# Kernel optimization log

Hardware: AMD Instinct MI355X
Metric: run time of the kernel (lower is better)

Reference implementation:

```python
import jax, jax.numpy as jnp
import numpy as np

M = 19
DIM = 768
D = DIM // 2  # r=2 -> 384
EPS = 1e-5


def _bn_eval(h, gamma, beta):
    # eval-mode BatchNorm1d with running_mean=0, running_var=1
    return h * (gamma / jnp.sqrt(1.0 + EPS)) + beta


def setup_inputs() -> dict:
    key = jax.random.key(0)
    ks = jax.random.split(key, 24)
    s = 0.02
    inp = {
        "x": jax.random.normal(ks[0], (4096, M * DIM), jnp.float32),
        "g": jax.random.normal(ks[1], (4096, M * DIM), jnp.float32),
        # fc: Linear(768,384) -> ReLU -> BN(384) -> Linear(384,384)
        "fc1_W": jax.random.normal(ks[2], (D, DIM), jnp.float32) * s,
        "fc1_b": jnp.zeros((D,), jnp.float32),
        "bn1_g": jnp.ones((D,), jnp.float32),
        "bn1_b": jnp.zeros((D,), jnp.float32),
        "fc2_W": jax.random.normal(ks[3], (D, D), jnp.float32) * s,
        "fc2_b": jnp.zeros((D,), jnp.float32),
        # 19 branch Linears fcs: (d,d); g_fcs: (dim+d, dim)
        "fcs_W": jax.random.normal(ks[4], (M, D, D), jnp.float32) * s,
        "fcs_b": jnp.zeros((M, D), jnp.float32),
        "gfcs_W": jax.random.normal(ks[5], (M, DIM, DIM + D), jnp.float32) * s,
        "gfcs_b": jnp.zeros((M, DIM), jnp.float32),
        # classifier head (numpy_class=20 < 30): 768->128->32->20
        "l1_W": jax.random.normal(ks[6], (128, DIM), jnp.float32) * s,
        "l1_b": jnp.zeros((128,), jnp.float32),
        "bna_g": jnp.ones((128,), jnp.float32),
        "bna_b": jnp.zeros((128,), jnp.float32),
        "l2_W": jax.random.normal(ks[7], (32, 128), jnp.float32) * s,
        "l2_b": jnp.zeros((32,), jnp.float32),
        "bnb_g": jnp.ones((32,), jnp.float32),
        "bnb_b": jnp.zeros((32,), jnp.float32),
        "l3_W": jax.random.normal(ks[8], (20, 32), jnp.float32) * s,
        "l3_b": jnp.zeros((20,), jnp.float32),
    }
    return inp


def reference(x, g, fc1_W, fc1_b, bn1_g, bn1_b, fc2_W, fc2_b,
              fcs_W, fcs_b, gfcs_W, gfcs_b,
              l1_W, l1_b, bna_g, bna_b, l2_W, l2_b, bnb_g, bnb_b, l3_W, l3_b):
    bs = x.shape[0]
    x3 = x.reshape(bs, M, DIM)
    g3 = g.reshape(bs, M, DIM)

    # selective_ts_with_g
    fea_u = jnp.sum(x3, axis=1)                              # (bs, 768)
    h = jax.nn.relu(fea_u @ fc1_W.T + fc1_b)
    h = _bn_eval(h, bn1_g, bn1_b)
    fea_z = h @ fc2_W.T + fc2_b                              # (bs, 384)

    # 19 branch small GEMMs, batched
    vec = jnp.einsum('bd,mod->bmo', fea_z, fcs_W) + fcs_b    # (bs, 19, 384)
    cat = jnp.concatenate([vec, g3], axis=-1)                # (bs, 19, 1152)
    att = jnp.einsum('bmi,moi->bmo', cat, gfcs_W) + gfcs_b   # (bs, 19, 768)
    att = jax.nn.softmax(att, axis=1)                        # softmax over 19 branches
    fea_v = jnp.sum(x3 * att, axis=1)                        # (bs, 768)

    # classifier head
    h = jax.nn.relu(fea_v @ l1_W.T + l1_b)
    h = _bn_eval(h, bna_g, bna_b)
    h = jax.nn.relu(h @ l2_W.T + l2_b)
    h = _bn_eval(h, bnb_g, bnb_b)
    return h @ l3_W.T + l3_b                                 # (bs, 20)
```

## Files before the change

### kernel.cpp

```cpp
#include <hip/hip_runtime.h>


typedef unsigned short u16;
typedef unsigned int u32;
typedef long long i64;
typedef float f32x4 __attribute__((ext_vector_type(4)));
typedef __bf16 bf16x8 __attribute__((ext_vector_type(8)));

#define GPTR(p) ((const __attribute__((address_space(1))) void*)(p))
#define SPTR(p) ((__attribute__((address_space(3))) void*)(p))

__device__ __forceinline__ u16 f2bf(float f) {
    u32 u = __float_as_uint(f);
    u += 0x7fffu + ((u >> 16) & 1u);
    return (u16)(u >> 16);
}
__device__ __forceinline__ float bf2f(u16 h) {
    return __uint_as_float(((u32)h) << 16);
}
__device__ __forceinline__ u32 pk2(float a, float b) {
    return (u32)f2bf(a) | ((u32)f2bf(b) << 16);
}

#define BNRS 0.9999950000374997f

#define EPI_NONE    0
#define EPI_BIAS    1
#define EPI_RELU_BN 2

template <int EPI>
__global__ __launch_bounds__(256)
void gemm_bf16_kernel(const u16* __restrict__ A, i64 Abat, int lda,
                      const u16* __restrict__ B, i64 Bbat, int ldb,
                      const float* __restrict__ bias,
                      const float* __restrict__ bnG, const float* __restrict__ bnB,
                      u16* __restrict__ C, i64 Cbat, int ldc, int K)
{
    constexpr int BK = 32;
    __shared__ __align__(16) u16 lA[128 * BK];
    __shared__ __align__(16) u16 lB[128 * BK];

    const int z    = blockIdx.z;
    const int tid  = threadIdx.x;
    const int wave = tid >> 6;
    const int lane = tid & 63;
    const int bm   = blockIdx.x * 128;
    const int bn   = blockIdx.y * 128;
    const int wm   = (wave >> 1) * 64;
    const int wn   = (wave & 1) * 64;
    const int rl   = lane & 15;
    const int qk   = (lane >> 4) * 8;

    f32x4 acc[4][4] = {};

    const u16* Ab = A + (size_t)z * Abat + (size_t)bm * lda;
    const u16* Bb = B + (size_t)z * Bbat + (size_t)bn * ldb;

    for (int k0 = 0; k0 < K; k0 += BK) {
#pragma unroll
        for (int r = 0; r < 2; ++r) {
            const int c   = r * 256 + wave * 64 + lane;
            const int row = c >> 2;
            const int kc  = (c & 3) << 3;
            const u16* sa = Ab + (size_t)row * lda + (k0 + kc);
            const u16* sb = Bb + (size_t)row * ldb + (k0 + kc);
            __builtin_amdgcn_global_load_lds(GPTR(sa), SPTR(&lA[(r * 256 + wave * 64) * 8]), 16, 0, 0);
            __builtin_amdgcn_global_load_lds(GPTR(sb), SPTR(&lB[(r * 256 + wave * 64) * 8]), 16, 0, 0);
        }
        __syncthreads();

        bf16x8 af[4], bfr[4];
#pragma unroll
        for (int i = 0; i < 4; ++i) af[i]  = *(const bf16x8*)&lA[(wm + i * 16 + rl) * BK + qk];
#pragma unroll
        for (int j = 0; j < 4; ++j) bfr[j] = *(const bf16x8*)&lB[(wn + j * 16 + rl) * BK + qk];
#pragma unroll
        for (int i = 0; i < 4; ++i)
#pragma unroll
            for (int j = 0; j < 4; ++j)
                acc[i][j] = __builtin_amdgcn_mfma_f32_16x16x32_bf16(af[i], bfr[j], acc[i][j], 0, 0, 0);
        __syncthreads();
    }

    u16* Cb = C + (size_t)z * Cbat;
    const int q4 = (lane >> 4) * 4;
#pragma unroll
    for (int j = 0; j < 4; ++j) {
        const int col = bn + wn + j * 16 + rl;
        float bsv = 0.f, scl = 1.f, sft = 0.f;
        if constexpr (EPI != EPI_NONE) bsv = bias[col];
        if constexpr (EPI == EPI_RELU_BN) { scl = bnG[col] * BNRS; sft = bnB[col]; }
#pragma unroll
        for (int i = 0; i < 4; ++i) {
            const int row0 = bm + wm + i * 16 + q4;
#pragma unroll
            for (int r = 0; r < 4; ++r) {
                float v = acc[i][j][r];
                if constexpr (EPI != EPI_NONE) v += bsv;
                if constexpr (EPI == EPI_RELU_BN) v = fmaxf(v, 0.f) * scl + sft;
                Cb[(size_t)(row0 + r) * ldc + col] = f2bf(v);
            }
        }
    }
}

__global__ __launch_bounds__(256)
void att_gemm_a_kernel(const u16* __restrict__ feaz, const u16* __restrict__ gb,
                       const u16* __restrict__ W, const float* __restrict__ bc,
                       u16* __restrict__ att)
{
    constexpr int BK = 32, K = 1152;
    __shared__ __align__(16) u16 lA[128 * BK];
    __shared__ __align__(16) u16 lB[128 * BK];

    const int m    = blockIdx.z;
    const int tid  = threadIdx.x;
    const int wave = tid >> 6;
    const int lane = tid & 63;
    const int bm   = blockIdx.x * 128;
    const int bn   = blockIdx.y * 128;
    const int wm   = (wave >> 1) * 64;
    const int wn   = (wave & 1) * 64;
    const int rl   = lane & 15;
    const int qk   = (lane >> 4) * 8;

    f32x4 acc[4][4] = {};

    const u16* A1 = feaz + (size_t)bm * 384;
    const u16* A2 = gb + (size_t)bm * 14592 + m * 768;
    const u16* Bb = W + (size_t)m * 884736 + (size_t)bn * K;

    for (int k0 = 0; k0 < K; k0 += BK) {
#pragma unroll
        for (int r = 0; r < 2; ++r) {
            const int c   = r * 256 + wave * 64 + lane;
            const int row = c >> 2;
            const int kc  = (c & 3) << 3;
            const u16* sa = (k0 < 384)
                ? A1 + (size_t)row * 384 + (k0 + kc)
                : A2 + (size_t)row * 14592 + (k0 - 384 + kc);
            const u16* sb = Bb + (size_t)row * K + (k0 + kc);
            __builtin_amdgcn_global_load_lds(GPTR(sa), SPTR(&lA[(r * 256 + wave * 64) * 8]), 16, 0, 0);
            __builtin_amdgcn_global_load_lds(GPTR(sb), SPTR(&lB[(r * 256 + wave * 64) * 8]), 16, 0, 0);
        }
        __syncthreads();

        bf16x8 af[4], bfr[4];
#pragma unroll
        for (int i = 0; i < 4; ++i) af[i]  = *(const bf16x8*)&lA[(wm + i * 16 + rl) * BK + qk];
#pragma unroll
        for (int j = 0; j < 4; ++j) bfr[j] = *(const bf16x8*)&lB[(wn + j * 16 + rl) * BK + qk];
#pragma unroll
        for (int i = 0; i < 4; ++i)
#pragma unroll
            for (int j = 0; j < 4; ++j)
                acc[i][j] = __builtin_amdgcn_mfma_f32_16x16x32_bf16(af[i], bfr[j], acc[i][j], 0, 0, 0);
        __syncthreads();
    }

    const int q4 = (lane >> 4) * 4;
#pragma unroll
    for (int j = 0; j < 4; ++j) {
        const int col = bn + wn + j * 16 + rl;
        const float bsv = bc[m * 768 + col];
#pragma unroll
        for (int i = 0; i < 4; ++i) {
            const int row0 = bm + wm + i * 16 + q4;
#pragma unroll
            for (int r = 0; r < 4; ++r)
                att[(size_t)(row0 + r) * 14592 + m * 768 + col] = f2bf(acc[i][j][r] + bsv);
        }
    }
}

__global__ __launch_bounds__(256)
void att_gemm_b_kernel(const u16* __restrict__ feaz, const float* __restrict__ g,
                       const u16* __restrict__ W, const float* __restrict__ bc,
                       u16* __restrict__ att)
{
    constexpr int BK = 32, K = 1152;
    __shared__ __align__(16) u16 lA[128 * BK];
    __shared__ __align__(16) u16 lB[128 * BK];

    const int m    = blockIdx.z;
    const int tid  = threadIdx.x;
    const int wave = tid >> 6;
    const int lane = tid & 63;
    const int bm   = blockIdx.x * 128;
    const int bn   = blockIdx.y * 128;
    const int wm   = (wave >> 1) * 64;
    const int wn   = (wave & 1) * 64;
    const int rl   = lane & 15;
    const int qk   = (lane >> 4) * 8;

    f32x4 acc[4][4] = {};

    const u16* A1 = feaz + (size_t)bm * 384;
    const float* Ag = g + (size_t)bm * 14592 + m * 768;
    const u16* Bb = W + (size_t)m * 884736 + (size_t)bn * K;

    for (int k0 = 0; k0 < K; k0 += BK) {
        if (k0 < 384) {
#pragma unroll
            for (int r = 0; r < 2; ++r) {
                const int c   = r * 256 + wave * 64 + lane;
                const int row = c >> 2;
                const int kc  = (c & 3) << 3;
                const u16* sa = A1 + (size_t)row * 384 + (k0 + kc);
                __builtin_amdgcn_global_load_lds(GPTR(sa), SPTR(&lA[(r * 256 + wave * 64) * 8]), 16, 0, 0);
            }
        } else {
#pragma unroll
            for (int r = 0; r < 2; ++r) {
                const int c   = r * 256 + tid;
                const int row = c >> 2;
                const int kc  = (c & 3) << 3;
                const float* sf = Ag + (size_t)row * 14592 + (k0 - 384 + kc);
                const float4 f0 = *(const float4*)sf;
                const float4 f1 = *(const float4*)(sf + 4);
                uint4 pk;
                pk.x = pk2(f0.x, f0.y);  pk.y = pk2(f0.z, f0.w);
                pk.z = pk2(f1.x, f1.y);  pk.w = pk2(f1.z, f1.w);
                *(uint4*)&lA[c * 8] = pk;
            }
        }
#pragma unroll
        for (int r = 0; r < 2; ++r) {
            const int c   = r * 256 + wave * 64 + lane;
            const int row = c >> 2;
            const int kc  = (c & 3) << 3;
            const u16* sb = Bb + (size_t)row * K + (k0 + kc);
            __builtin_amdgcn_global_load_lds(GPTR(sb), SPTR(&lB[(r * 256 + wave * 64) * 8]), 16, 0, 0);
        }
        __syncthreads();

        bf16x8 af[4], bfr[4];
#pragma unroll
        for (int i = 0; i < 4; ++i) af[i]  = *(const bf16x8*)&lA[(wm + i * 16 + rl) * BK + qk];
#pragma unroll
        for (int j = 0; j < 4; ++j) bfr[j] = *(const bf16x8*)&lB[(wn + j * 16 + rl) * BK + qk];
#pragma unroll
        for (int i = 0; i < 4; ++i)
#pragma unroll
            for (int j = 0; j < 4; ++j)
                acc[i][j] = __builtin_amdgcn_mfma_f32_16x16x32_bf16(af[i], bfr[j], acc[i][j], 0, 0, 0);
        __syncthreads();
    }

    const int q4 = (lane >> 4) * 4;
#pragma unroll
    for (int j = 0; j < 4; ++j) {
        const int col = bn + wn + j * 16 + rl;
        const float bsv = bc[m * 768 + col];
#pragma unroll
        for (int i = 0; i < 4; ++i) {
            const int row0 = bm + wm + i * 16 + q4;
#pragma unroll
            for (int r = 0; r < 4; ++r)
                att[(size_t)(row0 + r) * 14592 + m * 768 + col] = f2bf(acc[i][j][r] + bsv);
        }
    }
}


__global__ __launch_bounds__(256)
void cvt_flat_kernel(const float* __restrict__ s0, const float* __restrict__ s1,
                     const float* __restrict__ s2,
                     u16* __restrict__ d0, u16* __restrict__ d1, u16* __restrict__ d2)
{
    const int i = blockIdx.x * 256 + threadIdx.x;
    const float* s; u16* d; int off;
    if (i < 36864)      { s = s0; d = d0; off = i; }
    else if (i < 55296) { s = s1; d = d1; off = i - 36864; }
    else                { s = s2; d = d2; off = i - 55296; }
    const float4 f0 = *(const float4*)(s + off * 8);
    const float4 f1 = *(const float4*)(s + off * 8 + 4);
    uint4 pk; pk.x = pk2(f0.x, f0.y); pk.y = pk2(f0.z, f0.w);
    pk.z = pk2(f1.x, f1.y); pk.w = pk2(f1.z, f1.w);
    *(uint4*)(d + off * 8) = pk;
}

__global__ __launch_bounds__(256)
void cvt_gfcs_kernel(const float* __restrict__ gfcs, u16* __restrict__ w1,
                     u16* __restrict__ geff)
{
    const int i = blockIdx.x * 256 + threadIdx.x;
    const int r = i / 144, c = i - r * 144;
    const float* s = gfcs + (size_t)r * 1152 + c * 8;
    const float4 f0 = *(const float4*)s;
    const float4 f1 = *(const float4*)(s + 4);
    uint4 pk; pk.x = pk2(f0.x, f0.y); pk.y = pk2(f0.z, f0.w);
    pk.z = pk2(f1.x, f1.y); pk.w = pk2(f1.z, f1.w);
    u16* d = (c < 48) ? (w1 + (size_t)r * 384 + c * 8)
                      : (geff + (size_t)r * 1152 + c * 8);
    *(uint4*)d = pk;
}

__global__ __launch_bounds__(256)
void cvt_fcsT_kernel(const float* __restrict__ fcs, u16* __restrict__ fcswT)
{
    const int i = blockIdx.x * 256 + threadIdx.x;
    const int m = i / 18432, rem = i - m * 18432;
    const int d = rem / 48, e8 = (rem - d * 48) * 8;
    const float* s = fcs + (size_t)m * 147456 + (size_t)e8 * 384 + d;
    float f[8];
#pragma unroll
    for (int j = 0; j < 8; ++j) f[j] = s[j * 384];
    uint4 pk; pk.x = pk2(f[0], f[1]); pk.y = pk2(f[2], f[3]);
    pk.z = pk2(f[4], f[5]); pk.w = pk2(f[6], f[7]);
    *(uint4*)(fcswT + (size_t)m * 147456 + (size_t)d * 384 + e8) = pk;
}

__global__ __launch_bounds__(256)
void cvt_g_kernel(const float* __restrict__ g, u16* __restrict__ gb)
{
    const size_t i = ((size_t)blockIdx.x * 256 + threadIdx.x) * 8;
    const float4 f0 = *(const float4*)(g + i);
    const float4 f1 = *(const float4*)(g + i + 4);
    uint4 pk; pk.x = pk2(f0.x, f0.y); pk.y = pk2(f0.z, f0.w);
    pk.z = pk2(f1.x, f1.y); pk.w = pk2(f1.z, f1.w);
    *(uint4*)(gb + i) = pk;
}

__global__ __launch_bounds__(256)
void bc_kernel(const float* __restrict__ gfcs, const float* __restrict__ gfcs_b,
               const float* __restrict__ fcs_b, float* __restrict__ bc)
{
    const int widx = blockIdx.x * 4 + (threadIdx.x >> 6);
    const int lane = threadIdx.x & 63;
    const int m = widx / 768, o = widx - m * 768;
    const float* wr = gfcs + (size_t)m * 884736 + (size_t)o * 1152;
    const float* fb = fcs_b + m * 384;
    float a = 0.f;
#pragma unroll
    for (int t = 0; t < 6; ++t) a += wr[lane + t * 64] * fb[lane + t * 64];
#pragma unroll
    for (int off = 32; off > 0; off >>= 1) a += __shfl_down(a, off, 64);
    if (lane == 0) bc[widx] = gfcs_b[widx] + a;
}

__global__ __launch_bounds__(192)
void feau_kernel(const float* __restrict__ x, u16* __restrict__ feau)
{
    const int b = blockIdx.x;
    const int o = threadIdx.x * 4;
    const float* xp = x + (size_t)b * 14592 + o;
    float4 s = {0.f, 0.f, 0.f, 0.f};
#pragma unroll
    for (int m = 0; m < 19; ++m) {
        const float4 v = *(const float4*)(xp + m * 768);
        s.x += v.x; s.y += v.y; s.z += v.z; s.w += v.w;
    }
    ushort4 r; r.x = f2bf(s.x); r.y = f2bf(s.y); r.z = f2bf(s.z); r.w = f2bf(s.w);
    *(ushort4*)(feau + (size_t)b * 768 + o) = r;
}

__global__ __launch_bounds__(192)
void softmax_feav_kernel(const u16* __restrict__ att, const float* __restrict__ x,
                         u16* __restrict__ feav)
{
    const int b = blockIdx.x;
    const int o = threadIdx.x * 4;
    const u16* ap   = att + (size_t)b * 14592 + o;
    const float* xp = x   + (size_t)b * 14592 + o;
    float4 l[19];
    float4 mx = {-1e30f, -1e30f, -1e30f, -1e30f};
#pragma unroll
    for (int m = 0; m < 19; ++m) {
        const ushort4 u = *(const ushort4*)(ap + m * 768);
        l[m].x = bf2f(u.x); l[m].y = bf2f(u.y); l[m].z = bf2f(u.z); l[m].w = bf2f(u.w);
        mx.x = fmaxf(mx.x, l[m].x); mx.y = fmaxf(mx.y, l[m].y);
        mx.z = fmaxf(mx.z, l[m].z); mx.w = fmaxf(mx.w, l[m].w);
    }
    float4 s = {0.f, 0.f, 0.f, 0.f};
#pragma unroll
    for (int m = 0; m < 19; ++m) {
        l[m].x = __expf(l[m].x - mx.x); s.x += l[m].x;
        l[m].y = __expf(l[m].y - mx.y); s.y += l[m].y;
        l[m].z = __expf(l[m].z - mx.z); s.z += l[m].z;
        l[m].w = __expf(l[m].w - mx.w); s.w += l[m].w;
    }
    const float4 inv = {1.f / s.x, 1.f / s.y, 1.f / s.z, 1.f / s.w};
    float4 a = {0.f, 0.f, 0.f, 0.f};
#pragma unroll
    for (int m = 0; m < 19; ++m) {
        const float4 v = *(const float4*)(xp + m * 768);
        a.x += v.x * l[m].x; a.y += v.y * l[m].y;
        a.z += v.z * l[m].z; a.w += v.w * l[m].w;
    }
    ushort4 r;
    r.x = f2bf(a.x * inv.x); r.y = f2bf(a.y * inv.y);
    r.z = f2bf(a.z * inv.z); r.w = f2bf(a.w * inv.w);
    *(ushort4*)(feav + (size_t)b * 768 + o) = r;
}

__global__ __launch_bounds__(256)
void l2_kernel(const u16* __restrict__ h1, const float* __restrict__ W,
               const float* __restrict__ bias, const float* __restrict__ bg,
               const float* __restrict__ bb, float* __restrict__ h2)
{
    const int idx = blockIdx.x * 256 + threadIdx.x;
    const int b = idx >> 5, n = idx & 31;
    const u16* hp  = h1 + (size_t)b * 128;
    const float* wp = W + n * 128;
    float a = bias[n];
#pragma unroll 8
    for (int k = 0; k < 128; ++k) a += bf2f(hp[k]) * wp[k];
    a = fmaxf(a, 0.f) * (bg[n] * BNRS) + bb[n];
    h2[idx] = a;
}

__global__ __launch_bounds__(256)
void l3_kernel(const float* __restrict__ h2, const float* __restrict__ W,
               const float* __restrict__ bias, float* __restrict__ out)
{
    const int idx = blockIdx.x * 256 + threadIdx.x;
    const int b = idx / 20, n = idx - b * 20;
    const float* hp = h2 + (size_t)b * 32;
    const float* wp = W + n * 32;
    float a = bias[n];
#pragma unroll
    for (int k = 0; k < 32; ++k) a += hp[k] * wp[k];
    out[idx] = a;
}

extern "C" void kernel_launch(void* const* d_in, const int* in_sizes, int n_in,
                              void* d_out, int out_size, void* d_ws, size_t ws_size,
                              hipStream_t stream)
{
    const float* x      = (const float*)d_in[0];
    const float* g      = (const float*)d_in[1];
    const float* fc1_W  = (const float*)d_in[2];
    const float* fc1_b  = (const float*)d_in[3];
    const float* bn1_g  = (const float*)d_in[4];
    const float* bn1_b  = (const float*)d_in[5];
    const float* fc2_W  = (const float*)d_in[6];
    const float* fc2_b  = (const float*)d_in[7];
    const float* fcs_W  = (const float*)d_in[8];
    const float* fcs_b  = (const float*)d_in[9];
    const float* gfcs_W = (const float*)d_in[10];
    const float* gfcs_b = (const float*)d_in[11];
    const float* l1_W   = (const float*)d_in[12];
    const float* l1_b   = (const float*)d_in[13];
    const float* bna_g  = (const float*)d_in[14];
    const float* bna_b  = (const float*)d_in[15];
    const float* l2_W   = (const float*)d_in[16];
    const float* l2_b   = (const float*)d_in[17];
    const float* bnb_g  = (const float*)d_in[18];
    const float* bnb_b  = (const float*)d_in[19];
    const float* l3_W   = (const float*)d_in[20];
    const float* l3_b   = (const float*)d_in[21];
    float* out = (float*)d_out;
    (void)in_sizes; (void)n_in; (void)out_size;

    char* w = (char*)d_ws;
    size_t off = 0;
    auto alloc = [&](size_t bytes) { void* p = w + off; off += (bytes + 255) & ~(size_t)255; return p; };
    u16* fc1w  = (u16*)alloc(294912ull * 2);
    u16* fc2w  = (u16*)alloc(147456ull * 2);
    u16* l1w   = (u16*)alloc(98304ull * 2);
    u16* fcswT = (u16*)alloc(2801664ull * 2);
    u16* w1bf  = (u16*)alloc(5603328ull * 2);
    u16* geff  = (u16*)alloc(16809984ull * 2);
    float* bcb = (float*)alloc(14592ull * 4);
    u16* feau  = (u16*)alloc(3145728ull * 2);
    u16* hbuf  = (u16*)alloc(1572864ull * 2);
    u16* feaz  = (u16*)alloc(1572864ull * 2);
    u16* attb  = (u16*)alloc(59768832ull * 2);
    u16* feav  = (u16*)alloc(3145728ull * 2);
    u16* h1b   = (u16*)alloc(524288ull * 2);
    float* h2f = (float*)alloc(131072ull * 4);
    u16* gbf   = (u16*)alloc(59768832ull * 2);
    const bool useA = (ws_size >= off);

    cvt_flat_kernel<<<264, 256, 0, stream>>>(fc1_W, fc2_W, l1_W, fc1w, fc2w, l1w);
    cvt_gfcs_kernel<<<8208, 256, 0, stream>>>(gfcs_W, w1bf, geff);
    cvt_fcsT_kernel<<<1368, 256, 0, stream>>>(fcs_W, fcswT);
    bc_kernel<<<3648, 256, 0, stream>>>(gfcs_W, gfcs_b, fcs_b, bcb);
    gemm_bf16_kernel<EPI_NONE><<<dim3(6, 3, 19), 256, 0, stream>>>(
        w1bf, 294912, 384, fcswT, 147456, 384, nullptr, nullptr, nullptr,
        geff, 884736, 1152, 384);
    if (useA) cvt_g_kernel<<<29184, 256, 0, stream>>>(g, gbf);

    feau_kernel<<<4096, 192, 0, stream>>>(x, feau);
    gemm_bf16_kernel<EPI_RELU_BN><<<dim3(32, 3), 256, 0, stream>>>(
        feau, 0, 768, fc1w, 0, 768, fc1_b, bn1_g, bn1_b, hbuf, 0, 384, 768);
    gemm_bf16_kernel<EPI_BIAS><<<dim3(32, 3), 256, 0, stream>>>(
        hbuf, 0, 384, fc2w, 0, 384, fc2_b, nullptr, nullptr, feaz, 0, 384, 384);

    if (useA)
        att_gemm_a_kernel<<<dim3(32, 6, 19), 256, 0, stream>>>(feaz, gbf, geff, bcb, attb);
    else
        att_gemm_b_kernel<<<dim3(32, 6, 19), 256, 0, stream>>>(feaz, g, geff, bcb, attb);
    softmax_feav_kernel<<<4096, 192, 0, stream>>>(attb, x, feav);

    gemm_bf16_kernel<EPI_RELU_BN><<<dim3(32, 1), 256, 0, stream>>>(
        feav, 0, 768, l1w, 0, 768, l1_b, bna_g, bna_b, h1b, 0, 128, 768);
    l2_kernel<<<512, 256, 0, stream>>>(h1b, l2_W, l2_b, bnb_g, bnb_b, h2f);
    l3_kernel<<<320, 256, 0, stream>>>(h2f, l3_W, l3_b, out);
}
```

Before: 930.6 us.

## Fuse g fp32-to-bf16 conversion into attention GEMM via async LDS loads

Drops the separate pass that converts g to a bf16 workspace copy. The attention GEMM now loads raw fp32 g tiles into LDS with async global-to-LDS loads and converts them to bf16 while building MFMA fragments. This removes one full read and write of the 4096x14592 g tensor, at the cost of a larger LDS footprint and conversion work inside the GEMM loop. It also replaces the fcs transpose with an LDS-tiled transpose and fuses the l2 and l3 head layers into a single kernel.

```diff
diff --git a/kernel.cpp b/kernel.cpp
--- a/kernel.cpp
+++ b/kernel.cpp
@@ -105,13 +105,14 @@
 }
 
 __global__ __launch_bounds__(256)
-void att_gemm_a_kernel(const u16* __restrict__ feaz, const u16* __restrict__ gb,
-                       const u16* __restrict__ W, const float* __restrict__ bc,
-                       u16* __restrict__ att)
+void att_gemm_kernel(const u16* __restrict__ feaz, const float* __restrict__ g,
+                     const u16* __restrict__ W, const float* __restrict__ bc,
+                     u16* __restrict__ att)
 {
     constexpr int BK = 32, K = 1152;
     __shared__ __align__(16) u16 lA[128 * BK];
     __shared__ __align__(16) u16 lB[128 * BK];
+    __shared__ __align__(16) float lG[128 * BK];
 
     const int m    = blockIdx.z;
     const int tid  = threadIdx.x;
@@ -126,78 +127,9 @@
 
     f32x4 acc[4][4] = {};
 
-    const u16* A1 = feaz + (size_t)bm * 384;
-    const u16* A2 = gb + (size_t)bm * 14592 + m * 768;
-    const u16* Bb = W + (size_t)m * 884736 + (size_t)bn * K;
-
-    for (int k0 = 0; k0 < K; k0 += BK) {
-#pragma unroll
-        for (int r = 0; r < 2; ++r) {
-            const int c   = r * 256 + wave * 64 + lane;
-            const int row = c >> 2;
-            const int kc  = (c & 3) << 3;
-            const u16* sa = (k0 < 384)
-                ? A1 + (size_t)row * 384 + (k0 + kc)
-                : A2 + (size_t)row * 14592 + (k0 - 384 + kc);
-            const u16* sb = Bb + (size_t)row * K + (k0 + kc);
-            __builtin_amdgcn_global_load_lds(GPTR(sa), SPTR(&lA[(r * 256 + wave * 64) * 8]), 16, 0, 0);
-            __builtin_amdgcn_global_load_lds(GPTR(sb), SPTR(&lB[(r * 256 + wave * 64) * 8]), 16, 0, 0);
-        }
-        __syncthreads();
-
-        bf16x8 af[4], bfr[4];
-#pragma unroll
-        for (int i = 0; i < 4; ++i) af[i]  = *(const bf16x8*)&lA[(wm + i * 16 + rl) * BK + qk];
-#pragma unroll
-        for (int j = 0; j < 4; ++j) bfr[j] = *(const bf16x8*)&lB[(wn + j * 16 + rl) * BK + qk];
-#pragma unroll
-        for (int i = 0; i < 4; ++i)
-#pragma unroll
-            for (int j = 0; j < 4; ++j)
-                acc[i][j] = __builtin_amdgcn_mfma_f32_16x16x32_bf16(af[i], bfr[j], acc[i][j], 0, 0, 0);
-        __syncthreads();
-    }
-
-    const int q4 = (lane >> 4) * 4;
-#pragma unroll
-    for (int j = 0; j < 4; ++j) {
-        const int col = bn + wn + j * 16 + rl;
-        const float bsv = bc[m * 768 + col];
-#pragma unroll
-        for (int i = 0; i < 4; ++i) {
-            const int row0 = bm + wm + i * 16 + q4;
-#pragma unroll
-            for (int r = 0; r < 4; ++r)
-                att[(size_t)(row0 + r) * 14592 + m * 768 + col] = f2bf(acc[i][j][r] + bsv);
-        }
-    }
-}
-
-__global__ __launch_bounds__(256)
-void att_gemm_b_kernel(const u16* __restrict__ feaz, const float* __restrict__ g,
-                       const u16* __restrict__ W, const float* __restrict__ bc,
-                       u16* __restrict__ att)
-{
-    constexpr int BK = 32, K = 1152;
-    __shared__ __align__(16) u16 lA[128 * BK];
-    __shared__ __align__(16) u16 lB[128 * BK];
-
-    const int m    = blockIdx.z;
-    const int tid  = threadIdx.x;
-    const int wave = tid >> 6;
-    const int lane = tid & 63;
-    const int bm   = blockIdx.x * 128;
-    const int bn   = blockIdx.y * 128;
-    const int wm   = (wave >> 1) * 64;
-    const int wn   = (wave & 1) * 64;
-    const int rl   = lane & 15;
-    const int qk   = (lane >> 4) * 8;
-
-    f32x4 acc[4][4] = {};
-
-    const u16* A1 = feaz + (size_t)bm * 384;
+    const u16*  A1 = feaz + (size_t)bm * 384;
     const float* Ag = g + (size_t)bm * 14592 + m * 768;
-    const u16* Bb = W + (size_t)m * 884736 + (size_t)bn * K;
+    const u16*  Bb = W + (size_t)m * 884736 + (size_t)bn * K;
 
     for (int k0 = 0; k0 < K; k0 += BK) {
         if (k0 < 384) {
@@ -211,17 +143,12 @@
             }
         } else {
 #pragma unroll
-            for (int r = 0; r < 2; ++r) {
-                const int c   = r * 256 + tid;
-                const int row = c >> 2;
-                const int kc  = (c & 3) << 3;
-                const float* sf = Ag + (size_t)row * 14592 + (k0 - 384 + kc);
-                const float4 f0 = *(const float4*)sf;
-                const float4 f1 = *(const float4*)(sf + 4);
-                uint4 pk;
-                pk.x = pk2(f0.x, f0.y);  pk.y = pk2(f0.z, f0.w);
-                pk.z = pk2(f1.x, f1.y);  pk.w = pk2(f1.z, f1.w);
-                *(uint4*)&lA[c * 8] = pk;
+            for (int r = 0; r < 4; ++r) {
+                const int c   = r * 256 + wave * 64 + lane;
+                const int row = c >> 3;
+                const int kc  = (c & 7) << 2;
+                const float* sg = Ag + (size_t)row * 14592 + (k0 - 384 + kc);
+                __builtin_amdgcn_global_load_lds(GPTR(sg), SPTR(&lG[(r * 256 + wave * 64) * 4]), 16, 0, 0);
             }
         }
 #pragma unroll
@@ -235,8 +162,21 @@
         __syncthreads();
 
         bf16x8 af[4], bfr[4];
-#pragma unroll
-        for (int i = 0; i < 4; ++i) af[i]  = *(const bf16x8*)&lA[(wm + i * 16 + rl) * BK + qk];
+        if (k0 < 384) {
+#pragma unroll
+            for (int i = 0; i < 4; ++i) af[i] = *(const bf16x8*)&lA[(wm + i * 16 + rl) * BK + qk];
+        } else {
+#pragma unroll
+            for (int i = 0; i < 4; ++i) {
+                const float* p = &lG[(wm + i * 16 + rl) * BK + qk];
+                const float4 p0 = *(const float4*)p;
+                const float4 p1 = *(const float4*)(p + 4);
+                union { bf16x8 v; uint4 u; } cv;
+                cv.u.x = pk2(p0.x, p0.y); cv.u.y = pk2(p0.z, p0.w);
+                cv.u.z = pk2(p1.x, p1.y); cv.u.w = pk2(p1.z, p1.w);
+                af[i] = cv.v;
+            }
+        }
 #pragma unroll
         for (int j = 0; j < 4; ++j) bfr[j] = *(const bf16x8*)&lB[(wn + j * 16 + rl) * BK + qk];
 #pragma unroll
@@ -297,29 +237,33 @@
 }
 
 __global__ __launch_bounds__(256)
-void cvt_fcsT_kernel(const float* __restrict__ fcs, u16* __restrict__ fcswT)
-{
-    const int i = blockIdx.x * 256 + threadIdx.x;
-    const int m = i / 18432, rem = i - m * 18432;
-    const int d = rem / 48, e8 = (rem - d * 48) * 8;
-    const float* s = fcs + (size_t)m * 147456 + (size_t)e8 * 384 + d;
-    float f[8];
-#pragma unroll
-    for (int j = 0; j < 8; ++j) f[j] = s[j * 384];
-    uint4 pk; pk.x = pk2(f[0], f[1]); pk.y = pk2(f[2], f[3]);
-    pk.z = pk2(f[4], f[5]); pk.w = pk2(f[6], f[7]);
-    *(uint4*)(fcswT + (size_t)m * 147456 + (size_t)d * 384 + e8) = pk;
-}
-
-__global__ __launch_bounds__(256)
-void cvt_g_kernel(const float* __restrict__ g, u16* __restrict__ gb)
-{
-    const size_t i = ((size_t)blockIdx.x * 256 + threadIdx.x) * 8;
-    const float4 f0 = *(const float4*)(g + i);
-    const float4 f1 = *(const float4*)(g + i + 4);
-    uint4 pk; pk.x = pk2(f0.x, f0.y); pk.y = pk2(f0.z, f0.w);
-    pk.z = pk2(f1.x, f1.y); pk.w = pk2(f1.z, f1.w);
-    *(uint4*)(gb + i) = pk;
+void fcsT_kernel(const float* __restrict__ fcs, u16* __restrict__ fcswT)
+{
+    __shared__ float t[64][65];
+    const int m  = blockIdx.z;
+    const int e0 = blockIdx.x * 64;
+    const int d0 = blockIdx.y * 64;
+    const int tr = threadIdx.x >> 4;
+    const int tc = (threadIdx.x & 15) * 4;
+
+    const float* src = fcs + (size_t)m * 147456 + (size_t)e0 * 384 + d0;
+#pragma unroll
+    for (int rr = 0; rr < 4; ++rr) {
+        const int e = rr * 16 + tr;
+        const float4 v = *(const float4*)(src + (size_t)e * 384 + tc);
+        t[e][tc] = v.x; t[e][tc + 1] = v.y; t[e][tc + 2] = v.z; t[e][tc + 3] = v.w;
+    }
+    __syncthreads();
+
+    u16* dst = fcswT + (size_t)m * 147456 + (size_t)d0 * 384 + e0;
+#pragma unroll
+    for (int rr = 0; rr < 4; ++rr) {
+        const int d = rr * 16 + tr;
+        ushort4 o;
+        o.x = f2bf(t[tc + 0][d]); o.y = f2bf(t[tc + 1][d]);
+        o.z = f2bf(t[tc + 2][d]); o.w = f2bf(t[tc + 3][d]);
+        *(ushort4*)(dst + (size_t)d * 384 + tc) = o;
+    }
 }
 
 __global__ __launch_bounds__(256)
@@ -395,33 +339,29 @@
 }
 
 __global__ __launch_bounds__(256)
-void l2_kernel(const u16* __restrict__ h1, const float* __restrict__ W,
-               const float* __restrict__ bias, const float* __restrict__ bg,
-               const float* __restrict__ bb, float* __restrict__ h2)
-{
-    const int idx = blockIdx.x * 256 + threadIdx.x;
-    const int b = idx >> 5, n = idx & 31;
-    const u16* hp  = h1 + (size_t)b * 128;
-    const float* wp = W + n * 128;
-    float a = bias[n];
-#pragma unroll 8
-    for (int k = 0; k < 128; ++k) a += bf2f(hp[k]) * wp[k];
-    a = fmaxf(a, 0.f) * (bg[n] * BNRS) + bb[n];
-    h2[idx] = a;
-}
-
-__global__ __launch_bounds__(256)
-void l3_kernel(const float* __restrict__ h2, const float* __restrict__ W,
-               const float* __restrict__ bias, float* __restrict__ out)
-{
-    const int idx = blockIdx.x * 256 + threadIdx.x;
-    const int b = idx / 20, n = idx - b * 20;
-    const float* hp = h2 + (size_t)b * 32;
-    const float* wp = W + n * 32;
-    float a = bias[n];
-#pragma unroll
-    for (int k = 0; k < 32; ++k) a += hp[k] * wp[k];
-    out[idx] = a;
+void head23_kernel(const u16* __restrict__ h1, const float* __restrict__ l2W,
+                   const float* __restrict__ l2b, const float* __restrict__ bg,
+                   const float* __restrict__ bb, const float* __restrict__ l3W,
+                   const float* __restrict__ l3b, float* __restrict__ out)
+{
+    const int b    = blockIdx.x * 4 + (threadIdx.x >> 6);
+    const int lane = threadIdx.x & 63;
+    const int n    = lane & 31;
+    const int half = lane >> 5;
+    const u16* hp  = h1 + (size_t)b * 128 + half * 64;
+    const float* wp = l2W + n * 128 + half * 64;
+    float a = 0.f;
+#pragma unroll
+    for (int k = 0; k < 64; ++k) a += bf2f(hp[k]) * wp[k];
+    a += __shfl_xor(a, 32, 64);
+    float h2 = fmaxf(a + l2b[n], 0.f) * (bg[n] * BNRS) + bb[n];
+    float o = 0.f;
+#pragma unroll
+    for (int nn = 0; nn < 32; ++nn) {
+        const float v = __shfl(h2, nn, 64);
+        if (lane < 20) o += v * l3W[lane * 32 + nn];
+    }
+    if (lane < 20) out[(size_t)b * 20 + lane] = o + l3b[lane];
 }
 
 extern "C" void kernel_launch(void* const* d_in, const int* in_sizes, int n_in,
@@ -451,7 +391,7 @@
     const float* l3_W   = (const float*)d_in[20];
     const float* l3_b   = (const float*)d_in[21];
     float* out = (float*)d_out;
-    (void)in_sizes; (void)n_in; (void)out_size;
+    (void)in_sizes; (void)n_in; (void)out_size; (void)ws_size;
 
     char* w = (char*)d_ws;
     size_t off = 0;
@@ -469,18 +409,14 @@
     u16* attb  = (u16*)alloc(59768832ull * 2);
     u16* feav  = (u16*)alloc(3145728ull * 2);
     u16* h1b   = (u16*)alloc(524288ull * 2);
-    float* h2f = (float*)alloc(131072ull * 4);
-    u16* gbf   = (u16*)alloc(59768832ull * 2);
-    const bool useA = (ws_size >= off);
 
     cvt_flat_kernel<<<264, 256, 0, stream>>>(fc1_W, fc2_W, l1_W, fc1w, fc2w, l1w);
     cvt_gfcs_kernel<<<8208, 256, 0, stream>>>(gfcs_W, w1bf, geff);
-    cvt_fcsT_kernel<<<1368, 256, 0, stream>>>(fcs_W, fcswT);
+    fcsT_kernel<<<dim3(6, 6, 19), 256, 0, stream>>>(fcs_W, fcswT);
     bc_kernel<<<3648, 256, 0, stream>>>(gfcs_W, gfcs_b, fcs_b, bcb);
     gemm_bf16_kernel<EPI_NONE><<<dim3(6, 3, 19), 256, 0, stream>>>(
         w1bf, 294912, 384, fcswT, 147456, 384, nullptr, nullptr, nullptr,
         geff, 884736, 1152, 384);
-    if (useA) cvt_g_kernel<<<29184, 256, 0, stream>>>(g, gbf);
 
     feau_kernel<<<4096, 192, 0, stream>>>(x, feau);
     gemm_bf16_kernel<EPI_RELU_BN><<<dim3(32, 3), 256, 0, stream>>>(
@@ -488,14 +424,10 @@
     gemm_bf16_kernel<EPI_BIAS><<<dim3(32, 3), 256, 0, stream>>>(
         hbuf, 0, 384, fc2w, 0, 384, fc2_b, nullptr, nullptr, feaz, 0, 384, 384);
 
-    if (useA)
-        att_gemm_a_kernel<<<dim3(32, 6, 19), 256, 0, stream>>>(feaz, gbf, geff, bcb, attb);
-    else
-        att_gemm_b_kernel<<<dim3(32, 6, 19), 256, 0, stream>>>(feaz, g, geff, bcb, attb);
+    att_gemm_kernel<<<dim3(32, 6, 19), 256, 0, stream>>>(feaz, g, geff, bcb, attb);
     softmax_feav_kernel<<<4096, 192, 0, stream>>>(attb, x, feav);
 
     gemm_bf16_kernel<EPI_RELU_BN><<<dim3(32, 1), 256, 0, stream>>>(
         feav, 0, 768, l1w, 0, 768, l1_b, bna_g, bna_b, h1b, 0, 128, 768);
-    l2_kernel<<<512, 256, 0, stream>>>(h1b, l2_W, l2_b, bnb_g, bnb_b, h2f);
-    l3_kernel<<<320, 256, 0, stream>>>(h2f, l3_W, l3_b, out);
-}
+    head23_kernel<<<1024, 256, 0, stream>>>(h1b, l2_W, l2_b, bnb_g, bnb_b, l3_W, l3_b, out);
+}
```

Result: slower. 1.005 ms (+8.0%).
